# Kernel optimization log

Measured on AMD Instinct MI355X. Metric: run time of the kernel, lower is better.

The kernel has to match this reference:

```python
import jax, jax.numpy as jnp
import numpy as np

# Constants matching module_cfg
H, W = 256, 256          # cfg.img_size
N_GAUSS, CF = 1024, 15   # number of Gaussians, appearance feature channels (feat_dim-1)


def setup_inputs() -> dict:
    key = jax.random.key(0)
    k0, k1, k2, k3, k4 = jax.random.split(key, 5)
    # Gaussians in front of an identity camera (z in [2,4])
    xy = jax.random.normal(k0, (N_GAUSS, 2), dtype=jnp.float32) * 0.5
    z = jax.random.uniform(k1, (N_GAUSS, 1), minval=2.0, maxval=4.0, dtype=jnp.float32)
    xyzs = jnp.concatenate([xy, z], axis=-1)[None]                      # [1,N,3]
    feats = jax.random.uniform(k2, (1, N_GAUSS, CF), dtype=jnp.float32)  # [1,N,15]
    opac = jax.random.uniform(k3, (1, N_GAUSS, 1), minval=0.3, maxval=0.9, dtype=jnp.float32)
    # PSD 3D covariances (small splats)
    A = jax.random.normal(k4, (N_GAUSS, 3, 3), dtype=jnp.float32) * 0.02
    cov = (jnp.einsum('nij,nkj->nik', A, A) + 1e-4 * jnp.eye(3, dtype=jnp.float32))[None]  # [1,N,3,3]
    fx = fy = 500.0
    K = jnp.array([[[fx, 0.0, W / 2.0], [0.0, fy, H / 2.0], [0.0, 0.0, 1.0]]], dtype=jnp.float32)
    E = jnp.eye(4, dtype=jnp.float32)[None]  # world-to-camera
    return {"xyzs_observation": xyzs, "appearance_feats": feats, "opacity": opac,
            "cov": cov, "K": K, "E": E}


def _render(xyzs, feats, opac, cov, K, E):
    """Fused 3DGS rasterization: geometry/sort computed once, all channels composited in one pass
    (the original loops the full pipeline per 3-channel slice)."""
    fx, fy = K[0, 0, 0], K[0, 1, 1]
    px, py = K[0, 0, 2], K[0, 1, 2]
    R = E[0, :3, :3]
    tr = E[0, :3, 3]
    p = xyzs[0]                      # [N,3] world
    t = p @ R.T + tr                 # [N,3] camera space
    tz = t[:, 2]
    # EWA Jacobian with frustum clamping (as in 3DGS computeCov2D)
    limx = 1.3 * (W / (2.0 * fx))    # 1.3 * tanfovx
    limy = 1.3 * (H / (2.0 * fy))
    txc = jnp.clip(t[:, 0] / tz, -limx, limx) * tz
    tyc = jnp.clip(t[:, 1] / tz, -limy, limy) * tz
    z2 = tz * tz
    zeros = jnp.zeros_like(tz)
    J = jnp.stack([jnp.stack([fx / tz, zeros, -fx * txc / z2], -1),
                   jnp.stack([zeros, fy / tz, -fy * tyc / z2], -1)], -2)  # [N,2,3]
    Tm = J @ R                                                           # [N,2,3]
    c2 = jnp.einsum('nij,njk,nlk->nil', Tm, cov[0], Tm)                  # [N,2,2]
    a = c2[:, 0, 0] + 0.3  # low-pass dilation as in 3DGS
    b = c2[:, 0, 1]
    c = c2[:, 1, 1] + 0.3
    det = a * c - b * b
    inv = 1.0 / det
    cA, cB, cC = c * inv, -b * inv, a * inv                              # conic
    # projected pixel-space means (NDC->pixel as in 3DGS: fx*x/z + px - 0.5)
    ux = fx * t[:, 0] / tz + px - 0.5
    uy = fy * t[:, 1] / tz + py - 0.5
    valid = (tz > 0.2) & (det > 0.0)  # frustum / degenerate cull
    # feat = [appearance, ones] -> last channel renders accumulated alpha
    feat = jnp.concatenate([feats[0], jnp.ones_like(opac[0])], axis=-1)  # [N,C]
    op = jnp.where(valid, opac[0, :, 0], 0.0)
    # global front-to-back depth sort
    order = jnp.argsort(tz)
    ux, uy, cA, cB, cC, op = (v[order] for v in (ux, uy, cA, cB, cC, op))
    feat = feat[order]
    # pixel grid (integer pixel coords, as in the CUDA kernel)
    yg, xg = jnp.meshgrid(jnp.arange(H, dtype=jnp.float32),
                          jnp.arange(W, dtype=jnp.float32), indexing='ij')
    xg = xg.reshape(-1)  # [P]
    yg = yg.reshape(-1)
    dx = ux[None, :] - xg[:, None]   # [P,N]
    dy = uy[None, :] - yg[:, None]
    power = -0.5 * (cA[None, :] * dx * dx + cC[None, :] * dy * dy) - cB[None, :] * dx * dy
    g = jnp.where(power <= 0.0, jnp.exp(jnp.minimum(power, 0.0)), 0.0)
    alpha = jnp.minimum(0.99, op[None, :] * g)
    alpha = jnp.where(alpha < 1.0 / 255.0, 0.0, alpha)  # per-splat cull as in kernel
    trans = jnp.cumprod(1.0 - alpha, axis=1)
    Tprev = jnp.concatenate([jnp.ones((alpha.shape[0], 1), alpha.dtype), trans[:, :-1]], axis=1)
    wgt = Tprev * alpha              # [P,N] compositing weights
    img = wgt @ feat                 # [P,C]  all channels in one pass (bg = 0)
    img = img.reshape(H, W, -1)[None]  # [1,H,W,C]
    return img[..., :-1], img[..., -1]


def reference(xyzs_observation, appearance_feats, opacity, cov, K, E):
    return _render(xyzs_observation, appearance_feats, opacity, cov, K, E)
```

## Files before the change

### kernel.cpp

```cpp
#include <hip/hip_runtime.h>
#include <math.h>

#define HH 256
#define WW 256
#define NG 1024
#define CF 15

extern "C" __global__ __launch_bounds__(1024)
void geom_sort_kernel(const float* __restrict__ xyz,
                      const float* __restrict__ feats,
                      const float* __restrict__ opac,
                      const float* __restrict__ cov,
                      const float* __restrict__ Kp,
                      const float* __restrict__ Ep,
                      float4* __restrict__ g0,
                      float4* __restrict__ g1,
                      float4* __restrict__ cullv,
                      float4* __restrict__ feat_s)
{
    __shared__ float sg[9][NG];
    __shared__ unsigned long long skey[NG];

    const int i = threadIdx.x;

    const float fx = Kp[0], px = Kp[2], fy = Kp[4], py = Kp[5];
    const float R00 = Ep[0], R01 = Ep[1], R02 = Ep[2],  tr0 = Ep[3];
    const float R10 = Ep[4], R11 = Ep[5], R12 = Ep[6],  tr1 = Ep[7];
    const float R20 = Ep[8], R21 = Ep[9], R22 = Ep[10], tr2 = Ep[11];

    const float p0 = xyz[i * 3 + 0], p1 = xyz[i * 3 + 1], p2 = xyz[i * 3 + 2];
    const float t0 = R00 * p0 + R01 * p1 + R02 * p2 + tr0;
    const float t1 = R10 * p0 + R11 * p1 + R12 * p2 + tr1;
    const float tz = R20 * p0 + R21 * p1 + R22 * p2 + tr2;

    const float limx = 1.3f * ((float)WW / (2.0f * fx));
    const float limy = 1.3f * ((float)HH / (2.0f * fy));
    const float itz = 1.0f / tz;
    const float txz = t0 * itz, tyz = t1 * itz;
    const float txc = fminf(fmaxf(txz, -limx), limx) * tz;
    const float tyc = fminf(fmaxf(tyz, -limy), limy) * tz;
    const float z2 = tz * tz;
    const float J00 = fx * itz, J02 = -fx * txc / z2;
    const float J11 = fy * itz, J12 = -fy * tyc / z2;

    const float T00 = J00 * R00 + J02 * R20;
    const float T01 = J00 * R01 + J02 * R21;
    const float T02 = J00 * R02 + J02 * R22;
    const float T10 = J11 * R10 + J12 * R20;
    const float T11 = J11 * R11 + J12 * R21;
    const float T12 = J11 * R12 + J12 * R22;

    const float* C = cov + i * 9;
    const float c00 = C[0], c01 = C[1], c02 = C[2];
    const float c10 = C[3], c11 = C[4], c12 = C[5];
    const float c20 = C[6], c21 = C[7], c22 = C[8];

    const float M00 = T00 * c00 + T01 * c10 + T02 * c20;
    const float M01 = T00 * c01 + T01 * c11 + T02 * c21;
    const float M02 = T00 * c02 + T01 * c12 + T02 * c22;
    const float M10 = T10 * c00 + T11 * c10 + T12 * c20;
    const float M11 = T10 * c01 + T11 * c11 + T12 * c21;
    const float M12 = T10 * c02 + T11 * c12 + T12 * c22;

    const float A2 = M00 * T00 + M01 * T01 + M02 * T02 + 0.3f;
    const float B2 = M00 * T10 + M01 * T11 + M02 * T12;
    const float C2 = M10 * T10 + M11 * T11 + M12 * T12 + 0.3f;

    const float det = A2 * C2 - B2 * B2;
    const float inv = 1.0f / det;
    const float cA = C2 * inv, cB = -B2 * inv, cC = A2 * inv;

    const float ux = fx * txz + px - 0.5f;
    const float uy = fy * tyz + py - 0.5f;

    const bool valid = (tz > 0.2f) && (det > 0.0f);
    const float op = valid ? opac[i] : 0.0f;
    const float pthr = (op > 0.0f) ? logf(1.0f / (255.0f * op)) : 3.0e38f;

    float bx = -1.0e30f, by = -1.0e30f;
    if (op > 0.0f) {
        const float L = -2.0f * pthr;
        bx = sqrtf(L * A2);
        by = sqrtf(L * C2);
    }

    sg[0][i] = ux;
    sg[1][i] = uy;
    sg[2][i] = -0.5f * cA;
    sg[3][i] = -cB;
    sg[4][i] = -0.5f * cC;
    sg[5][i] = op;
    sg[6][i] = pthr;
    sg[7][i] = bx;
    sg[8][i] = by;

    unsigned u = __float_as_uint(tz);
    u = (u & 0x80000000u) ? ~u : (u | 0x80000000u);
    unsigned long long key = ((unsigned long long)u << 32) | (unsigned)i;

    __syncthreads();

    for (int k = 2; k <= NG; k <<= 1) {
        for (int j = k >> 1; j > 0; j >>= 1) {
            const bool up = ((i & k) == 0);
            const bool lower = ((i & j) == 0);
            unsigned long long part;
            if (j >= 64) {
                skey[i] = key;
                __syncthreads();
                part = skey[i ^ j];
                __syncthreads();
            } else {
                part = __shfl_xor(key, j);
            }
            const bool takeMin = (up == lower);
            const bool partSmaller = (part < key);
            key = (takeMin == partSmaller) ? part : key;
        }
    }

    const int s = (int)(unsigned)(key & 0xffffffffull);

    g0[i]    = make_float4(sg[0][s], sg[1][s], sg[2][s], sg[3][s]);
    g1[i]    = make_float4(sg[4][s], sg[5][s], sg[6][s], 0.0f);
    cullv[i] = make_float4(sg[0][s], sg[1][s], sg[7][s], sg[8][s]);

    const float* f = feats + s * CF;
    feat_s[i * 4 + 0] = make_float4(f[0],  f[1],  f[2],  f[3]);
    feat_s[i * 4 + 1] = make_float4(f[4],  f[5],  f[6],  f[7]);
    feat_s[i * 4 + 2] = make_float4(f[8],  f[9],  f[10], f[11]);
    feat_s[i * 4 + 3] = make_float4(f[12], f[13], f[14], 1.0f);
}

extern "C" __global__ __launch_bounds__(256)
void render_kernel(const float4* __restrict__ g0,
                   const float4* __restrict__ g1,
                   const float4* __restrict__ cullv,
                   const float4* __restrict__ feat_s,
                   float* __restrict__ out0,
                   float* __restrict__ out1)
{
    __shared__ float4 sA[256];
    __shared__ float4 sB[256];
    __shared__ float4 sF[256][4];
    __shared__ int wcnt[4];

    const int tid = threadIdx.x;
    const int tx = blockIdx.x & 15, ty = blockIdx.x >> 4;
    const int x0 = tx * 16, y0 = ty * 16;
    const int x = x0 + (tid & 15);
    const int y = y0 + (tid >> 4);
    const float xf = (float)x, yf = (float)y;
    const float tlx = (float)x0, thx = (float)(x0 + 15);
    const float tly = (float)y0, thy = (float)(y0 + 15);

    float T = 1.0f;
    float acc[16];
#pragma unroll
    for (int c = 0; c < 16; ++c) acc[c] = 0.0f;

    for (int c = 0; c < NG / 256; ++c) {
        if (__syncthreads_and(T < 1e-4f)) break;

        const int g = c * 256 + tid;
        const float4 cu = cullv[g];
        const bool hit = (cu.x + cu.z >= tlx) && (cu.x - cu.z <= thx) &&
                         (cu.y + cu.w >= tly) && (cu.y - cu.w <= thy);

        const unsigned long long bal = __ballot(hit);
        const int lane = tid & 63, w = tid >> 6;
        if (lane == 0) wcnt[w] = __popcll(bal);
        __syncthreads();

        int base = 0;
#pragma unroll
        for (int q = 0; q < 4; ++q) base += (q < w) ? wcnt[q] : 0;
        const int cnt = wcnt[0] + wcnt[1] + wcnt[2] + wcnt[3];

        if (hit) {
            const int slot = base + __popcll(bal & ((1ull << lane) - 1ull));
            sA[slot] = g0[g];
            sB[slot] = g1[g];
            sF[slot][0] = feat_s[(g << 2) + 0];
            sF[slot][1] = feat_s[(g << 2) + 1];
            sF[slot][2] = feat_s[(g << 2) + 2];
            sF[slot][3] = feat_s[(g << 2) + 3];
        }
        __syncthreads();

        for (int e = 0; e < cnt; ++e) {
            const float4 a = sA[e];
            const float4 b = sB[e];
            const float dx = a.x - xf;
            const float dy = a.y - yf;
            float power = a.z * dx * dx;
            power = fmaf(a.w, dx * dy, power);
            power = fmaf(b.x, dy * dy, power);
            if (power <= 0.0f && power >= b.z) {
                const float alpha = fminf(0.99f, b.y * __expf(power));
                const float wgt = T * alpha;
                const float4 f0 = sF[e][0];
                const float4 f1 = sF[e][1];
                const float4 f2 = sF[e][2];
                const float4 f3 = sF[e][3];
                acc[0]  = fmaf(wgt, f0.x, acc[0]);
                acc[1]  = fmaf(wgt, f0.y, acc[1]);
                acc[2]  = fmaf(wgt, f0.z, acc[2]);
                acc[3]  = fmaf(wgt, f0.w, acc[3]);
                acc[4]  = fmaf(wgt, f1.x, acc[4]);
                acc[5]  = fmaf(wgt, f1.y, acc[5]);
                acc[6]  = fmaf(wgt, f1.z, acc[6]);
                acc[7]  = fmaf(wgt, f1.w, acc[7]);
                acc[8]  = fmaf(wgt, f2.x, acc[8]);
                acc[9]  = fmaf(wgt, f2.y, acc[9]);
                acc[10] = fmaf(wgt, f2.z, acc[10]);
                acc[11] = fmaf(wgt, f2.w, acc[11]);
                acc[12] = fmaf(wgt, f3.x, acc[12]);
                acc[13] = fmaf(wgt, f3.y, acc[13]);
                acc[14] = fmaf(wgt, f3.z, acc[14]);
                acc[15] = fmaf(wgt, f3.w, acc[15]);
                T *= (1.0f - alpha);
            }
        }
    }

    const int pix = y * WW + x;
#pragma unroll
    for (int c = 0; c < CF; ++c) out0[pix * CF + c] = acc[c];
    out1[pix] = acc[15];
}

extern "C" void kernel_launch(void* const* d_in, const int* in_sizes, int n_in,
                              void* d_out, int out_size, void* d_ws, size_t ws_size,
                              hipStream_t stream) {
    const float* xyz   = (const float*)d_in[0];
    const float* feats = (const float*)d_in[1];
    const float* opac  = (const float*)d_in[2];
    const float* cov   = (const float*)d_in[3];
    const float* Kp    = (const float*)d_in[4];
    const float* Ep    = (const float*)d_in[5];

    float* ws = (float*)d_ws;
    float4* g0     = (float4*)ws;
    float4* g1     = (float4*)(ws + NG * 4);
    float4* cullv  = (float4*)(ws + NG * 8);
    float4* feat_s = (float4*)(ws + NG * 12);

    geom_sort_kernel<<<1, NG, 0, stream>>>(xyz, feats, opac, cov, Kp, Ep,
                                           g0, g1, cullv, feat_s);

    float* out0 = (float*)d_out;
    float* out1 = out0 + HH * WW * CF;
    render_kernel<<<256, 256, 0, stream>>>(g0, g1, cullv, feat_s, out0, out1);
}
```

Baseline: 91.26 us.

## Fuse geometry and sort into render kernel with per-tile culled bitonic sort

Removes the single-block geometry/sort kernel and its workspace round trip. Each tile block now recomputes the projection for all Gaussians, culls them against its own tile, and bitonic-sorts only the surviving keys in shared memory. It then recomputes the geometry for the sorted survivors while loading them into shared memory. The change removes one launch and a serial 1024-thread sort, at the cost of redundant geometry math in every block, an extra geometry pass per survivor, and sort time that grows with each tile's hit count. It also adds an early exit every 32 splats once every lane in the wave is saturated.

```diff
diff --git a/kernel.cpp b/kernel.cpp
--- a/kernel.cpp
+++ b/kernel.cpp
@@ -6,27 +6,22 @@
 #define NG 1024
 #define CF 15
 
-extern "C" __global__ __launch_bounds__(1024)
-void geom_sort_kernel(const float* __restrict__ xyz,
-                      const float* __restrict__ feats,
-                      const float* __restrict__ opac,
-                      const float* __restrict__ cov,
-                      const float* __restrict__ Kp,
-                      const float* __restrict__ Ep,
-                      float4* __restrict__ g0,
-                      float4* __restrict__ g1,
-                      float4* __restrict__ cullv,
-                      float4* __restrict__ feat_s)
+struct G {
+    float ux, uy, hA, hB, hC, op, pthr, bx, by;
+    unsigned kz;
+};
+
+__device__ __forceinline__ G geom(int i,
+                                  const float* __restrict__ xyz,
+                                  const float* __restrict__ opac,
+                                  const float* __restrict__ cov,
+                                  const float* __restrict__ s )
 {
-    __shared__ float sg[9][NG];
-    __shared__ unsigned long long skey[NG];
-
-    const int i = threadIdx.x;
-
-    const float fx = Kp[0], px = Kp[2], fy = Kp[4], py = Kp[5];
-    const float R00 = Ep[0], R01 = Ep[1], R02 = Ep[2],  tr0 = Ep[3];
-    const float R10 = Ep[4], R11 = Ep[5], R12 = Ep[6],  tr1 = Ep[7];
-    const float R20 = Ep[8], R21 = Ep[9], R22 = Ep[10], tr2 = Ep[11];
+    const float fx = s[0], fy = s[1], px = s[2], py = s[3];
+    const float R00 = s[4],  R01 = s[5],  R02 = s[6];
+    const float R10 = s[7],  R11 = s[8],  R12 = s[9];
+    const float R20 = s[10], R21 = s[11], R22 = s[12];
+    const float tr0 = s[13], tr1 = s[14], tr2 = s[15];
 
     const float p0 = xyz[i * 3 + 0], p1 = xyz[i * 3 + 1], p2 = xyz[i * 3 + 2];
     const float t0 = R00 * p0 + R01 * p1 + R02 * p2 + tr0;
@@ -51,16 +46,12 @@
     const float T12 = J11 * R12 + J12 * R22;
 
     const float* C = cov + i * 9;
-    const float c00 = C[0], c01 = C[1], c02 = C[2];
-    const float c10 = C[3], c11 = C[4], c12 = C[5];
-    const float c20 = C[6], c21 = C[7], c22 = C[8];
-
-    const float M00 = T00 * c00 + T01 * c10 + T02 * c20;
-    const float M01 = T00 * c01 + T01 * c11 + T02 * c21;
-    const float M02 = T00 * c02 + T01 * c12 + T02 * c22;
-    const float M10 = T10 * c00 + T11 * c10 + T12 * c20;
-    const float M11 = T10 * c01 + T11 * c11 + T12 * c21;
-    const float M12 = T10 * c02 + T11 * c12 + T12 * c22;
+    const float M00 = T00 * C[0] + T01 * C[3] + T02 * C[6];
+    const float M01 = T00 * C[1] + T01 * C[4] + T02 * C[7];
+    const float M02 = T00 * C[2] + T01 * C[5] + T02 * C[8];
+    const float M10 = T10 * C[0] + T11 * C[3] + T12 * C[6];
+    const float M11 = T10 * C[1] + T11 * C[4] + T12 * C[7];
+    const float M12 = T10 * C[2] + T11 * C[5] + T12 * C[8];
 
     const float A2 = M00 * T00 + M01 * T01 + M02 * T02 + 0.3f;
     const float B2 = M00 * T10 + M01 * T11 + M02 * T12;
@@ -70,161 +61,175 @@
     const float inv = 1.0f / det;
     const float cA = C2 * inv, cB = -B2 * inv, cC = A2 * inv;
 
-    const float ux = fx * txz + px - 0.5f;
-    const float uy = fy * tyz + py - 0.5f;
+    G r;
+    r.ux = fx * txz + px - 0.5f;
+    r.uy = fy * tyz + py - 0.5f;
+    r.hA = -0.5f * cA;
+    r.hB = -cB;
+    r.hC = -0.5f * cC;
 
     const bool valid = (tz > 0.2f) && (det > 0.0f);
-    const float op = valid ? opac[i] : 0.0f;
-    const float pthr = (op > 0.0f) ? logf(1.0f / (255.0f * op)) : 3.0e38f;
-
-    float bx = -1.0e30f, by = -1.0e30f;
-    if (op > 0.0f) {
-        const float L = -2.0f * pthr;
-        bx = sqrtf(L * A2);
-        by = sqrtf(L * C2);
-    }
-
-    sg[0][i] = ux;
-    sg[1][i] = uy;
-    sg[2][i] = -0.5f * cA;
-    sg[3][i] = -cB;
-    sg[4][i] = -0.5f * cC;
-    sg[5][i] = op;
-    sg[6][i] = pthr;
-    sg[7][i] = bx;
-    sg[8][i] = by;
+    r.op = valid ? opac[i] : 0.0f;
+    r.pthr = (r.op > 0.0f) ? logf(1.0f / (255.0f * r.op)) : 3.0e38f;
+
+    if (r.op > 0.0f) {
+        const float L = -2.0f * r.pthr;
+        r.bx = sqrtf(L * A2);
+        r.by = sqrtf(L * C2);
+    } else {
+        r.bx = -1.0e30f;
+        r.by = -1.0e30f;
+    }
 
     unsigned u = __float_as_uint(tz);
-    u = (u & 0x80000000u) ? ~u : (u | 0x80000000u);
-    unsigned long long key = ((unsigned long long)u << 32) | (unsigned)i;
-
-    __syncthreads();
-
-    for (int k = 2; k <= NG; k <<= 1) {
-        for (int j = k >> 1; j > 0; j >>= 1) {
-            const bool up = ((i & k) == 0);
-            const bool lower = ((i & j) == 0);
-            unsigned long long part;
-            if (j >= 64) {
-                skey[i] = key;
-                __syncthreads();
-                part = skey[i ^ j];
-                __syncthreads();
-            } else {
-                part = __shfl_xor(key, j);
-            }
-            const bool takeMin = (up == lower);
-            const bool partSmaller = (part < key);
-            key = (takeMin == partSmaller) ? part : key;
-        }
-    }
-
-    const int s = (int)(unsigned)(key & 0xffffffffull);
-
-    g0[i]    = make_float4(sg[0][s], sg[1][s], sg[2][s], sg[3][s]);
-    g1[i]    = make_float4(sg[4][s], sg[5][s], sg[6][s], 0.0f);
-    cullv[i] = make_float4(sg[0][s], sg[1][s], sg[7][s], sg[8][s]);
-
-    const float* f = feats + s * CF;
-    feat_s[i * 4 + 0] = make_float4(f[0],  f[1],  f[2],  f[3]);
-    feat_s[i * 4 + 1] = make_float4(f[4],  f[5],  f[6],  f[7]);
-    feat_s[i * 4 + 2] = make_float4(f[8],  f[9],  f[10], f[11]);
-    feat_s[i * 4 + 3] = make_float4(f[12], f[13], f[14], 1.0f);
+    r.kz = (u & 0x80000000u) ? ~u : (u | 0x80000000u);
+    return r;
 }
 
-extern "C" __global__ __launch_bounds__(256)
-void render_kernel(const float4* __restrict__ g0,
-                   const float4* __restrict__ g1,
-                   const float4* __restrict__ cullv,
-                   const float4* __restrict__ feat_s,
-                   float* __restrict__ out0,
-                   float* __restrict__ out1)
+__global__ __launch_bounds__(256)
+void render_fused(const float* __restrict__ xyz,
+                  const float* __restrict__ feats,
+                  const float* __restrict__ opac,
+                  const float* __restrict__ cov,
+                  const float* __restrict__ Kp,
+                  const float* __restrict__ Ep,
+                  float* __restrict__ out0,
+                  float* __restrict__ out1)
 {
+    __shared__ float sKE[16];
+    __shared__ unsigned long long skey[NG];
     __shared__ float4 sA[256];
     __shared__ float4 sB[256];
     __shared__ float4 sF[256][4];
     __shared__ int wcnt[4];
 
     const int tid = threadIdx.x;
+
+    if (tid == 0) {
+        sKE[0]  = Kp[0]; sKE[1]  = Kp[4]; sKE[2]  = Kp[2]; sKE[3]  = Kp[5];
+        sKE[4]  = Ep[0]; sKE[5]  = Ep[1]; sKE[6]  = Ep[2];
+        sKE[7]  = Ep[4]; sKE[8]  = Ep[5]; sKE[9]  = Ep[6];
+        sKE[10] = Ep[8]; sKE[11] = Ep[9]; sKE[12] = Ep[10];
+        sKE[13] = Ep[3]; sKE[14] = Ep[7]; sKE[15] = Ep[11];
+    }
+    __syncthreads();
+
     const int tx = blockIdx.x & 15, ty = blockIdx.x >> 4;
     const int x0 = tx * 16, y0 = ty * 16;
-    const int x = x0 + (tid & 15);
-    const int y = y0 + (tid >> 4);
-    const float xf = (float)x, yf = (float)y;
+    const float xf = (float)(x0 + (tid & 15));
+    const float yf = (float)(y0 + (tid >> 4));
     const float tlx = (float)x0, thx = (float)(x0 + 15);
     const float tly = (float)y0, thy = (float)(y0 + 15);
+
+    int tot = 0;
+    for (int c = 0; c < NG / 256; ++c) {
+        const int g = c * 256 + tid;
+        const G gg = geom(g, xyz, opac, cov, sKE);
+        const bool hit = (gg.ux + gg.bx >= tlx) && (gg.ux - gg.bx <= thx) &&
+                         (gg.uy + gg.by >= tly) && (gg.uy - gg.by <= thy);
+
+        const unsigned long long bal = __ballot(hit);
+        const int lane = tid & 63, w = tid >> 6;
+        if (lane == 0) wcnt[w] = __popcll(bal);
+        __syncthreads();
+        int base = tot;
+#pragma unroll
+        for (int q = 0; q < 4; ++q) base += (q < w) ? wcnt[q] : 0;
+        if (hit) {
+            const int slot = base + __popcll(bal & ((1ull << lane) - 1ull));
+            skey[slot] = ((unsigned long long)gg.kz << 32) | (unsigned)g;
+        }
+        tot += wcnt[0] + wcnt[1] + wcnt[2] + wcnt[3];
+        __syncthreads();
+    }
 
     float T = 1.0f;
     float acc[16];
 #pragma unroll
     for (int c = 0; c < 16; ++c) acc[c] = 0.0f;
 
-    for (int c = 0; c < NG / 256; ++c) {
-        if (__syncthreads_and(T < 1e-4f)) break;
-
-        const int g = c * 256 + tid;
-        const float4 cu = cullv[g];
-        const bool hit = (cu.x + cu.z >= tlx) && (cu.x - cu.z <= thx) &&
-                         (cu.y + cu.w >= tly) && (cu.y - cu.w <= thy);
-
-        const unsigned long long bal = __ballot(hit);
-        const int lane = tid & 63, w = tid >> 6;
-        if (lane == 0) wcnt[w] = __popcll(bal);
+    if (tot > 0) {
+        int K = 1;
+        while (K < tot) K <<= 1;
+        for (int e = tot + tid; e < K; e += 256) skey[e] = ~0ull;
         __syncthreads();
 
-        int base = 0;
-#pragma unroll
-        for (int q = 0; q < 4; ++q) base += (q < w) ? wcnt[q] : 0;
-        const int cnt = wcnt[0] + wcnt[1] + wcnt[2] + wcnt[3];
-
-        if (hit) {
-            const int slot = base + __popcll(bal & ((1ull << lane) - 1ull));
-            sA[slot] = g0[g];
-            sB[slot] = g1[g];
-            sF[slot][0] = feat_s[(g << 2) + 0];
-            sF[slot][1] = feat_s[(g << 2) + 1];
-            sF[slot][2] = feat_s[(g << 2) + 2];
-            sF[slot][3] = feat_s[(g << 2) + 3];
-        }
-        __syncthreads();
-
-        for (int e = 0; e < cnt; ++e) {
-            const float4 a = sA[e];
-            const float4 b = sB[e];
-            const float dx = a.x - xf;
-            const float dy = a.y - yf;
-            float power = a.z * dx * dx;
-            power = fmaf(a.w, dx * dy, power);
-            power = fmaf(b.x, dy * dy, power);
-            if (power <= 0.0f && power >= b.z) {
-                const float alpha = fminf(0.99f, b.y * __expf(power));
-                const float wgt = T * alpha;
-                const float4 f0 = sF[e][0];
-                const float4 f1 = sF[e][1];
-                const float4 f2 = sF[e][2];
-                const float4 f3 = sF[e][3];
-                acc[0]  = fmaf(wgt, f0.x, acc[0]);
-                acc[1]  = fmaf(wgt, f0.y, acc[1]);
-                acc[2]  = fmaf(wgt, f0.z, acc[2]);
-                acc[3]  = fmaf(wgt, f0.w, acc[3]);
-                acc[4]  = fmaf(wgt, f1.x, acc[4]);
-                acc[5]  = fmaf(wgt, f1.y, acc[5]);
-                acc[6]  = fmaf(wgt, f1.z, acc[6]);
-                acc[7]  = fmaf(wgt, f1.w, acc[7]);
-                acc[8]  = fmaf(wgt, f2.x, acc[8]);
-                acc[9]  = fmaf(wgt, f2.y, acc[9]);
-                acc[10] = fmaf(wgt, f2.z, acc[10]);
-                acc[11] = fmaf(wgt, f2.w, acc[11]);
-                acc[12] = fmaf(wgt, f3.x, acc[12]);
-                acc[13] = fmaf(wgt, f3.y, acc[13]);
-                acc[14] = fmaf(wgt, f3.z, acc[14]);
-                acc[15] = fmaf(wgt, f3.w, acc[15]);
-                T *= (1.0f - alpha);
+        for (int k = 2; k <= K; k <<= 1) {
+            for (int j = k >> 1; j > 0; j >>= 1) {
+                for (int e = tid; e < K; e += 256) {
+                    const int ixj = e ^ j;
+                    if (ixj > e) {
+                        const unsigned long long a = skey[e];
+                        const unsigned long long b = skey[ixj];
+                        const bool up = ((e & k) == 0);
+                        if (up ? (a > b) : (a < b)) {
+                            skey[e] = b;
+                            skey[ixj] = a;
+                        }
+                    }
+                }
+                __syncthreads();
             }
         }
-    }
-
-    const int pix = y * WW + x;
+
+        const int nrun = (tot + 255) >> 8;
+        for (int run = 0; run < nrun; ++run) {
+            const int rbase = run << 8;
+            const int s = rbase + tid;
+            if (s < tot) {
+                const int idx = (int)(unsigned)(skey[s] & 0xffffffffull);
+                const G gg = geom(idx, xyz, opac, cov, sKE);
+                sA[tid] = make_float4(gg.ux, gg.uy, gg.hA, gg.hB);
+                sB[tid] = make_float4(gg.hC, gg.op, gg.pthr, 0.0f);
+                const float* f = feats + idx * CF;
+                sF[tid][0] = make_float4(f[0],  f[1],  f[2],  f[3]);
+                sF[tid][1] = make_float4(f[4],  f[5],  f[6],  f[7]);
+                sF[tid][2] = make_float4(f[8],  f[9],  f[10], f[11]);
+                sF[tid][3] = make_float4(f[12], f[13], f[14], 1.0f);
+            }
+            __syncthreads();
+
+            const int cnt = min(256, tot - rbase);
+            for (int e = 0; e < cnt; ++e) {
+                const float4 a = sA[e];
+                const float4 b = sB[e];
+                const float dx = a.x - xf;
+                const float dy = a.y - yf;
+                float power = a.z * dx * dx;
+                power = fmaf(a.w, dx * dy, power);
+                power = fmaf(b.x, dy * dy, power);
+                if (power <= 0.0f && power >= b.z) {
+                    const float alpha = fminf(0.99f, b.y * __expf(power));
+                    const float wgt = T * alpha;
+                    const float4 f0 = sF[e][0];
+                    const float4 f1 = sF[e][1];
+                    const float4 f2 = sF[e][2];
+                    const float4 f3 = sF[e][3];
+                    acc[0]  = fmaf(wgt, f0.x, acc[0]);
+                    acc[1]  = fmaf(wgt, f0.y, acc[1]);
+                    acc[2]  = fmaf(wgt, f0.z, acc[2]);
+                    acc[3]  = fmaf(wgt, f0.w, acc[3]);
+                    acc[4]  = fmaf(wgt, f1.x, acc[4]);
+                    acc[5]  = fmaf(wgt, f1.y, acc[5]);
+                    acc[6]  = fmaf(wgt, f1.z, acc[6]);
+                    acc[7]  = fmaf(wgt, f1.w, acc[7]);
+                    acc[8]  = fmaf(wgt, f2.x, acc[8]);
+                    acc[9]  = fmaf(wgt, f2.y, acc[9]);
+                    acc[10] = fmaf(wgt, f2.z, acc[10]);
+                    acc[11] = fmaf(wgt, f2.w, acc[11]);
+                    acc[12] = fmaf(wgt, f3.x, acc[12]);
+                    acc[13] = fmaf(wgt, f3.y, acc[13]);
+                    acc[14] = fmaf(wgt, f3.z, acc[14]);
+                    acc[15] = fmaf(wgt, f3.w, acc[15]);
+                    T *= (1.0f - alpha);
+                }
+                if ((e & 31) == 31 && __all(T < 1e-4f)) break;
+            }
+            if (__syncthreads_and(T < 1e-4f)) break;
+        }
+    }
+
+    const int pix = (y0 + (tid >> 4)) * WW + (x0 + (tid & 15));
 #pragma unroll
     for (int c = 0; c < CF; ++c) out0[pix * CF + c] = acc[c];
     out1[pix] = acc[15];
@@ -240,16 +245,9 @@
     const float* Kp    = (const float*)d_in[4];
     const float* Ep    = (const float*)d_in[5];
 
-    float* ws = (float*)d_ws;
-    float4* g0     = (float4*)ws;
-    float4* g1     = (float4*)(ws + NG * 4);
-    float4* cullv  = (float4*)(ws + NG * 8);
-    float4* feat_s = (float4*)(ws + NG * 12);
-
-    geom_sort_kernel<<<1, NG, 0, stream>>>(xyz, feats, opac, cov, Kp, Ep,
-                                           g0, g1, cullv, feat_s);
-
     float* out0 = (float*)d_out;
     float* out1 = out0 + HH * WW * CF;
-    render_kernel<<<256, 256, 0, stream>>>(g0, g1, cullv, feat_s, out0, out1);
+
+    render_fused<<<256, 256, 0, stream>>>(xyz, feats, opac, cov, Kp, Ep,
+                                          out0, out1);
 }
```

Measured after the change: 89.14 us. -2.3%, faster.
